# Kernel optimization log

Measured on AMD Instinct MI355X. Metric: run time of the kernel, lower is better.

Reference implementation:

```python
import jax, jax.numpy as jnp
import numpy as np

B, S, N = 16, 64, 4096
D = 64            # input_dim*seq_len == output_dim*graph_dim
FEAT = 64
E = 32768
HEADS = (3, 3, 1)
NEG_SLOPE = 0.2   # PyG GATConv default negative_slope


def _lin_init(key, fi, fo):
    k1, k2 = jax.random.split(key)
    s = 1.0 / np.sqrt(fi)
    return (jax.random.uniform(k1, (fi, fo), jnp.float32, -s, s),
            jax.random.uniform(k2, (fo,), jnp.float32, -s, s))


def setup_inputs() -> dict:
    key = jax.random.key(0)
    ks = jax.random.split(key, 32)
    inp = {}
    inp["inputs"] = jax.random.normal(ks[0], (B, S, N, 1), jnp.float32)
    inp["edge_index"] = jax.random.randint(ks[1], (2, E), 0, N, dtype=jnp.int32)
    inp["W_seq"], inp["b_seq"] = _lin_init(ks[2], D, D)
    inp["src_embed"] = jax.random.normal(ks[3], (N, FEAT), jnp.float32) * 0.1
    inp["tgt_embed"] = jax.random.normal(ks[4], (FEAT, N), jnp.float32) * 0.1
    for i, H in enumerate(HEADS):
        s = 1.0 / np.sqrt(D)
        inp[f"Wg{i}"] = jax.random.uniform(ks[5 + 5 * i], (D, H * D), jnp.float32, -s, s)
        inp[f"asrc{i}"] = jax.random.normal(ks[6 + 5 * i], (H, D), jnp.float32) * 0.1
        inp[f"adst{i}"] = jax.random.normal(ks[7 + 5 * i], (H, D), jnp.float32) * 0.1
        inp[f"bg{i}"] = jnp.zeros((D,), jnp.float32)
        inp[f"Wl{i}"], inp[f"bl{i}"] = _lin_init(ks[8 + 5 * i], D, D)
    inp["Wo"], inp["bo"] = _lin_init(ks[25], D, D)
    return inp


def _gat(x, src, dst, W, a_src, a_dst, b):
    # PyG GATConv, concat=False (mean over heads). x: [B,N,D] -> [B,N,D]
    H, C = a_src.shape
    xp = jnp.einsum('bnd,dhc->bnhc', x, W.reshape(D, H, C))       # [B,N,H,C]
    al_s = jnp.einsum('bnhc,hc->bnh', xp, a_src)
    al_d = jnp.einsum('bnhc,hc->bnh', xp, a_dst)
    e = jax.nn.leaky_relu(al_s[:, src] + al_d[:, dst], NEG_SLOPE)  # [B,Et,H]

    def per_graph(e_b, xj_b):
        m = jax.ops.segment_max(e_b, dst, num_segments=N)          # [N,H]
        w = jnp.exp(e_b - m[dst])
        z = jax.ops.segment_sum(w, dst, num_segments=N)
        alpha = w / z[dst]                                         # softmax per dst node
        return jax.ops.segment_sum(xj_b * alpha[..., None], dst, num_segments=N)

    out = jax.vmap(per_graph)(e, xp[:, src])                       # [B,N,H,C]
    return out.mean(axis=2) + b


def _forward(inputs, edge_index, W_seq, b_seq, src_embed, tgt_embed,
             Wg0, asrc0, adst0, bg0, Wl0, bl0,
             Wg1, asrc1, adst1, bg1, Wl1, bl1,
             Wg2, asrc2, adst2, bg2, Wl2, bl2, Wo, bo):
    loop = jnp.arange(N, dtype=edge_index.dtype)
    src = jnp.concatenate([edge_index[0], loop])   # PyG add_self_loops=True
    dst = jnp.concatenate([edge_index[1], loop])
    h = inputs.transpose(0, 2, 3, 1).reshape(B * N, D)
    h = h @ W_seq + b_seq + h                       # seq_linear residual
    A = jax.nn.softmax(jax.nn.relu(src_embed @ tgt_embed), axis=1)  # learned adjacency [N,N]
    gat_p = [(Wg0, asrc0, adst0, bg0), (Wg1, asrc1, adst1, bg1), (Wg2, asrc2, adst2, bg2)]
    lin_p = [(Wl0, bl0), (Wl1, bl1), (Wl2, bl2)]
    for i in range(3):
        hb = h.reshape(B, N, D)
        # layer-0 GAT output is computed but unused in the original code (dead); skip it
        h_cur = _gat(hb, src, dst, *gat_p[i]).reshape(B * N, D) if i > 0 else None
        adp = jnp.einsum('mn,bnd->bmd', A, hb)      # adaptive-graph matmul (dropout in eval = identity)
        adp = (adp @ lin_p[i][0] + lin_p[i][1]).reshape(B * N, D)
        g = jax.nn.sigmoid(adp)
        if i == 0:
            origin = h @ Wo + bo
            h = jnp.tanh(h) * g + origin * (1.0 - g)
        elif i == 1:
            h = jax.nn.leaky_relu(h_cur, 0.01) * g + h * (1.0 - g)
        else:
            h = jax.nn.relu(h_cur) * g + h * (1.0 - g)
    return h.reshape(B, N, 1, D)   # [batch, node_num, output_dim, graph_dim]


def reference(inputs, edge_index, W_seq, b_seq, src_embed, tgt_embed,
              Wg0, asrc0, adst0, bg0, Wl0, bl0,
              Wg1, asrc1, adst1, bg1, Wl1, bl1,
              Wg2, asrc2, adst2, bg2, Wl2, bl2, Wo, bo):
    return _forward(inputs, edge_index, W_seq, b_seq, src_embed, tgt_embed,
                    Wg0, asrc0, adst0, bg0, Wl0, bl0,
                    Wg1, asrc1, adst1, bg1, Wl1, bl1,
                    Wg2, asrc2, adst2, bg2, Wl2, bl2, Wo, bo)
```

## Files before the change

kernel.cpp:

```cpp
#include <hip/hip_runtime.h>
#include <stdint.h>

#define NB 16
#define NN 4096
#define DD 64
#define EE 32768
#define ETOT 36864
#define ROWS 65536
#define KSPLIT 4

typedef _Float16 f16;
typedef f16   half8 __attribute__((ext_vector_type(8)));
typedef f16   f16x8 __attribute__((ext_vector_type(8)));
typedef f16   f16x4 __attribute__((ext_vector_type(4)));
typedef float f32x4 __attribute__((ext_vector_type(4)));

__device__ __forceinline__ void gload16(const f16* g, f16* l) {
  __builtin_amdgcn_global_load_lds((const __attribute__((address_space(1))) void*)g,
                                   (__attribute__((address_space(3))) void*)l, 16, 0, 0);
}

__global__ __launch_bounds__(256) void k_zero2(int* a, int* b) {
  int i = blockIdx.x * 256 + threadIdx.x;
  if (i < NN) a[i] = 0;
  else if (i < 2 * NN) b[i - NN] = 0;
}

__global__ __launch_bounds__(256) void k_count(const int* __restrict__ ei, int* __restrict__ cnt) {
  int t = blockIdx.x * 256 + threadIdx.x;
  if (t >= ETOT) return;
  int d = (t < EE) ? ei[EE + t] : (t - EE);
  atomicAdd(&cnt[d], 1);
}

__global__ __launch_bounds__(256) void k_scan(const int* __restrict__ cnt, int* __restrict__ offs) {
  __shared__ int part[256];
  int t = threadIdx.x;
  int loc[16]; int s = 0;
  #pragma unroll
  for (int i = 0; i < 16; ++i) { int v = cnt[(t << 4) + i]; loc[i] = s; s += v; }
  part[t] = s;
  __syncthreads();
  int own = s;
  for (int d = 1; d < 256; d <<= 1) {
    int u = (t >= d) ? part[t - d] : 0;
    __syncthreads();
    part[t] += u;
    __syncthreads();
  }
  int base = part[t] - own;
  #pragma unroll
  for (int i = 0; i < 16; ++i) offs[(t << 4) + i] = base + loc[i];
}

__global__ __launch_bounds__(256) void k_fill(const int* __restrict__ ei, const int* __restrict__ offs,
                                              int* __restrict__ cur, int* __restrict__ esrc,
                                              int* __restrict__ edst) {
  int t = blockIdx.x * 256 + threadIdx.x;
  if (t >= ETOT) return;
  int s, d;
  if (t < EE) { s = ei[t]; d = ei[EE + t]; } else { s = d = t - EE; }
  int p = atomicAdd(&cur[d], 1);
  esrc[offs[d] + p] = s;
  edst[offs[d] + p] = d;
}

__global__ __launch_bounds__(256) void k_seq(const float* __restrict__ inp, const float* __restrict__ Wseq,
                                             const float* __restrict__ bseq, float* __restrict__ h) {
  __shared__ float X[64 * 68];
  int t = threadIdx.x;
  int b = blockIdx.x >> 6, n0 = (blockIdx.x & 63) << 6;
  #pragma unroll
  for (int i = 0; i < 16; ++i) {
    int idx = t + (i << 8);
    int s = idx >> 6, nl = idx & 63;
    X[nl * 68 + s] = inp[((size_t)((b << 6) + s) << 12) + n0 + nl];
  }
  __syncthreads();
  int c = t & 63, rg = t >> 6;
  float Wc[64];
  #pragma unroll
  for (int k = 0; k < 64; ++k) Wc[k] = Wseq[(k << 6) + c];
  float bc = bseq[c];
  for (int rr = 0; rr < 16; ++rr) {
    int r = (rg << 4) + rr;
    float a = bc + X[r * 68 + c];
    #pragma unroll
    for (int k4 = 0; k4 < 16; ++k4) {
      float4 x = *(const float4*)&X[r * 68 + (k4 << 2)];
      a = fmaf(x.x, Wc[4*k4+0], a); a = fmaf(x.y, Wc[4*k4+1], a);
      a = fmaf(x.z, Wc[4*k4+2], a); a = fmaf(x.w, Wc[4*k4+3], a);
    }
    h[((size_t)(b << 12) + n0 + r) * 64 + c] = a;
  }
}

__global__ __launch_bounds__(256) void k_adjmm(const f16* __restrict__ SEh, const f16* __restrict__ TEh,
                                               f16* __restrict__ A, float* __restrict__ Zpart) {
  __shared__ f16 Al[2][128 * 32];
  __shared__ f16 Bl[2][128 * 32];
  const int t = threadIdx.x, lane = t & 63, w = t >> 6;
  const int m0 = blockIdx.y << 7, j0 = blockIdx.x << 7;
  const int l15 = lane & 15, lhi = lane >> 4;
  const int wm = (w >> 1) << 6, wj = (w & 1) << 6;
  f32x4 acc[4][4] = {};
  const int c0 = (w << 6) + lane;
  const int row0 = c0 >> 2, ko0 = (c0 & 3) << 3;
  const int c1 = c0 + 256;
  const int row1 = c1 >> 2, ko1 = (c1 & 3) << 3;
  const f16* ga0 = SEh + (size_t)(m0 + row0) * 64 + ko0;
  const f16* ga1 = SEh + (size_t)(m0 + row1) * 64 + ko1;
  const f16* gb0 = TEh + (size_t)(j0 + row0) * 64 + ko0;
  const f16* gb1 = TEh + (size_t)(j0 + row1) * 64 + ko1;
  #pragma unroll
  for (int kt = 0; kt < 2; ++kt) {
    const int kof = kt << 5;
    gload16(ga0 + kof, Al[kt] + c0 * 8);
    gload16(ga1 + kof, Al[kt] + c1 * 8);
    gload16(gb0 + kof, Bl[kt] + c0 * 8);
    gload16(gb1 + kof, Bl[kt] + c1 * 8);
  }
  __syncthreads();
  #pragma unroll
  for (int kt = 0; kt < 2; ++kt) {
    half8 af[4], bf[4];
    #pragma unroll
    for (int i = 0; i < 4; ++i) {
      af[i] = *(const half8*)(Al[kt] + (wm + i * 16 + l15) * 32 + lhi * 8);
      bf[i] = *(const half8*)(Bl[kt] + (wj + i * 16 + l15) * 32 + lhi * 8);
    }
    #pragma unroll
    for (int mi = 0; mi < 4; ++mi)
      #pragma unroll
      for (int nj = 0; nj < 4; ++nj)
        acc[mi][nj] = __builtin_amdgcn_mfma_f32_16x16x32_f16(af[mi], bf[nj], acc[mi][nj], 0, 0, 0);
  }
  float rs[4][4];
  #pragma unroll
  for (int mi = 0; mi < 4; ++mi)
    #pragma unroll
    for (int r = 0; r < 4; ++r) rs[mi][r] = 0.f;
  #pragma unroll
  for (int mi = 0; mi < 4; ++mi)
    #pragma unroll
    for (int nj = 0; nj < 4; ++nj)
      #pragma unroll
      for (int r = 0; r < 4; ++r) {
        int row = m0 + wm + mi * 16 + lhi * 4 + r;
        int col = j0 + wj + nj * 16 + l15;
        float e = __expf(fmaxf(acc[mi][nj][r], 0.f));
        f16 eh = (f16)e;
        A[((size_t)row << 12) + col] = eh;
        rs[mi][r] += (float)eh;
      }
  #pragma unroll
  for (int mi = 0; mi < 4; ++mi)
    #pragma unroll
    for (int r = 0; r < 4; ++r) {
      float s = rs[mi][r];
      s += __shfl_xor(s, 1); s += __shfl_xor(s, 2);
      s += __shfl_xor(s, 4); s += __shfl_xor(s, 8);
      rs[mi][r] = s;
    }
  if (l15 == 0) {
    int p = (blockIdx.x << 1) + (w & 1);
    #pragma unroll
    for (int mi = 0; mi < 4; ++mi)
      #pragma unroll
      for (int r = 0; r < 4; ++r)
        Zpart[((size_t)p << 12) + m0 + wm + mi * 16 + lhi * 4 + r] = rs[mi][r];
  }
}

__global__ __launch_bounds__(256) void k_rowz(const float* __restrict__ Zpart, float* __restrict__ rowZ) {
  int row = blockIdx.x * 256 + threadIdx.x;
  float s = 0.f;
  #pragma unroll 8
  for (int p = 0; p < 64; ++p) s += Zpart[((size_t)p << 12) + row];
  rowZ[row] = 1.f / s;
}

#define NKT 16
__global__ __launch_bounds__(512) void k_gemm8(const f16* __restrict__ A, const f16* __restrict__ BT,
                                               f16* __restrict__ Cout) {
  extern __shared__ f16 smem[];
  const int t = threadIdx.x, lane = t & 63, wid = t >> 6;
  const int wr = wid >> 2, wc = wid & 3;
  const int l15 = lane & 15, lhi = lane >> 4;
  const int h7 = l15 & 7;
  const int wgid = blockIdx.x;
  const int nid = (wgid & 7) * 32 + (wgid >> 3);
  const int z = nid >> 6, rem = nid & 63;
  const int m0 = (rem >> 2) << 8;
  const int j0 = (rem & 3) << 8;
  const size_t kbase = (size_t)z << 10;
  f16* __restrict__ Cz = Cout + ((size_t)z << 22);

  const f16* gA[4]; int lA[4];
  #pragma unroll
  for (int i = 0; i < 4; ++i) {
    int s = t + (i << 9), row = s >> 3, sl = (s & 7) ^ (row & 7);
    gA[i] = A + (size_t)(m0 + row) * 4096 + kbase + sl * 8;
    lA[i] = s * 8;
  }
  const f16* gB[4]; int lB[4];
  #pragma unroll
  for (int i = 0; i < 4; ++i) {
    int s = t + (i << 9), row = s >> 3, sl = (s & 7) ^ (row & 7);
    gB[i] = BT + (size_t)(j0 + row) * 4096 + kbase + sl * 8;
    lB[i] = 16384 + s * 8;
  }
  #define SA(buf, kt, i) gload16(gA[i] + (kt) * 64, smem + (buf) * 32768 + lA[i])
  #define SB(buf, kt, i) gload16(gB[i] + (kt) * 64, smem + (buf) * 32768 + lB[i])

  const int rbase = wr << 7;
  const int cbase = wc << 6;
  f32x4 acc[8][4] = {};

  #pragma unroll
  for (int i = 0; i < 4; ++i) SA(0, 0, i);
  #pragma unroll
  for (int i = 0; i < 4; ++i) SB(0, 0, i);
  asm volatile("s_waitcnt vmcnt(0)" ::: "memory");
  __builtin_amdgcn_sched_barrier(0);
  __builtin_amdgcn_s_barrier();
  __builtin_amdgcn_sched_barrier(0);

  for (int kt = 0; kt < NKT; ++kt) {
    const int cur = kt & 1;
    const f16* Ab = smem + cur * 32768;
    const f16* Bb = Ab + 16384;
    const bool pf = (kt + 1 < NKT);
    {
      half8 af[8], bf[4];
      #pragma unroll
      for (int mi = 0; mi < 8; ++mi) {
        int row = rbase + mi * 16 + l15;
        af[mi] = *(const half8*)(Ab + row * 64 + (lhi ^ h7) * 8);
      }
      #pragma unroll
      for (int nj = 0; nj < 4; ++nj) {
        int row = cbase + nj * 16 + l15;
        bf[nj] = *(const half8*)(Bb + row * 64 + (lhi ^ h7) * 8);
      }
      if (pf) { SA(cur ^ 1, kt + 1, 0); SA(cur ^ 1, kt + 1, 1); SA(cur ^ 1, kt + 1, 2); SA(cur ^ 1, kt + 1, 3); }
      __builtin_amdgcn_s_setprio(1);
      #pragma unroll
      for (int mi = 0; mi < 8; ++mi)
        #pragma unroll
        for (int nj = 0; nj < 4; ++nj)
          acc[mi][nj] = __builtin_amdgcn_mfma_f32_16x16x32_f16(af[mi], bf[nj], acc[mi][nj], 0, 0, 0);
      __builtin_amdgcn_s_setprio(0);
    }
    {
      half8 af[8], bf[4];
      #pragma unroll
      for (int mi = 0; mi < 8; ++mi) {
        int row = rbase + mi * 16 + l15;
        af[mi] = *(const half8*)(Ab + row * 64 + ((4 + lhi) ^ h7) * 8);
      }
      #pragma unroll
      for (int nj = 0; nj < 4; ++nj) {
        int row = cbase + nj * 16 + l15;
        bf[nj] = *(const half8*)(Bb + row * 64 + ((4 + lhi) ^ h7) * 8);
      }
      if (pf) { SB(cur ^ 1, kt + 1, 0); SB(cur ^ 1, kt + 1, 1); SB(cur ^ 1, kt + 1, 2); SB(cur ^ 1, kt + 1, 3); }
      __builtin_amdgcn_s_setprio(1);
      #pragma unroll
      for (int mi = 0; mi < 8; ++mi)
        #pragma unroll
        for (int nj = 0; nj < 4; ++nj)
          acc[mi][nj] = __builtin_amdgcn_mfma_f32_16x16x32_f16(af[mi], bf[nj], acc[mi][nj], 0, 0, 0);
      __builtin_amdgcn_s_setprio(0);
    }
    if (pf) {
      asm volatile("s_waitcnt vmcnt(0)" ::: "memory");
      __builtin_amdgcn_sched_barrier(0);
      __builtin_amdgcn_s_barrier();
      __builtin_amdgcn_sched_barrier(0);
    }
  }
  #undef SA
  #undef SB
  #pragma unroll
  for (int mi = 0; mi < 8; ++mi)
    #pragma unroll
    for (int nj = 0; nj < 4; ++nj)
      #pragma unroll
      for (int r = 0; r < 4; ++r) {
        int row = m0 + rbase + mi * 16 + (lhi << 2) + r;
        int col = j0 + cbase + nj * 16 + l15;
        Cz[(size_t)row * 1024 + col] = (f16)acc[mi][nj][r];
      }
}

template<int H, int NP>
__device__ __forceinline__ void wprep_body(const float* __restrict__ Wg, const float* __restrict__ asrc,
                                           const float* __restrict__ adst, const float* __restrict__ Wl,
                                           f16* __restrict__ Wgh, int bid, int t) {
  const int WL0 = H * 64 + 16;
  for (int i = bid * 256 + t; i < NP * 64; i += 16 * 256) {
    int j = i >> 6, k = i & 63;
    float v;
    if (j < H * 64) {
      v = Wg[(size_t)k * (H * 64) + j];
    } else if (j < H * 64 + 2 * H) {
      int cc = j - H * 64, hh = cc >> 1;
      const float* a = ((cc & 1) ? adst : asrc) + (hh << 6);
      const float* wrow = Wg + (size_t)k * (H * 64) + (hh << 6);
      float s = 0.f;
      #pragma unroll 16
      for (int c = 0; c < 64; ++c) s = fmaf(wrow[c], a[c], s);
      v = s;
    } else if (j >= WL0 && j < WL0 + 64) {
      v = Wl[(k << 6) + (j - WL0)];
    } else v = 0.f;
    Wgh[(size_t)j * 64 + k] = (f16)v;
  }
}

__global__ __launch_bounds__(256) void k_allprep(
    const float* __restrict__ Wg1, const float* __restrict__ as1, const float* __restrict__ ad1,
    const float* __restrict__ Wl1, f16* __restrict__ Wgh1,
    const float* __restrict__ Wg2, const float* __restrict__ as2, const float* __restrict__ ad2,
    const float* __restrict__ Wl2, f16* __restrict__ Wgh2,
    const float* __restrict__ Wl0, const float* __restrict__ Wo, f16* __restrict__ W0h,
    const float* __restrict__ SE, const float* __restrict__ TE,
    f16* __restrict__ SEh, f16* __restrict__ TEh) {
  __shared__ float X[64 * 65];
  int bid = blockIdx.x, t = threadIdx.x;
  if (bid < 16) { wprep_body<3, 272>(Wg1, as1, ad1, Wl1, Wgh1, bid, t); return; }
  if (bid < 32) { wprep_body<1, 144>(Wg2, as2, ad2, Wl2, Wgh2, bid - 16, t); return; }
  if (bid < 40) {
    for (int i = (bid - 32) * 256 + t; i < 128 * 64; i += 8 * 256) {
      int j = i >> 6, k = i & 63;
      float v = (j < 64) ? Wl0[(k << 6) + j] : Wo[(k << 6) + (j - 64)];
      W0h[(size_t)j * 64 + k] = (f16)v;
    }
    return;
  }
  if (bid < 296) {
    int i = ((bid - 40) * 256 + t) * 4;
    float4 v = *(const float4*)(SE + i);
    f16 o[4] = {(f16)v.x, (f16)v.y, (f16)v.z, (f16)v.w};
    *(uint64_t*)(SEh + i) = *(uint64_t*)o;
    return;
  }
  int j0 = (bid - 296) << 6;
  #pragma unroll
  for (int i = 0; i < 16; ++i) {
    int idx = t + (i << 8);
    int k = idx >> 6, jl = idx & 63;
    X[jl * 65 + k] = TE[((size_t)k << 12) + j0 + jl];
  }
  __syncthreads();
  int jl = t >> 2, kg = t & 3;
  f16 o[16];
  #pragma unroll
  for (int i = 0; i < 16; ++i) o[i] = (f16)X[jl * 65 + (kg << 4) + i];
  f16* dst = TEh + ((size_t)(j0 + jl) << 6) + (kg << 4);
  *(uint64_t*)(dst + 0) = *(uint64_t*)(o + 0);
  *(uint64_t*)(dst + 4) = *(uint64_t*)(o + 4);
  *(uint64_t*)(dst + 8) = *(uint64_t*)(o + 8);
  *(uint64_t*)(dst + 12) = *(uint64_t*)(o + 12);
}

template<int H, int NP>
__global__ __launch_bounds__(256) void k_xpmm(const float* __restrict__ h, const f16* __restrict__ Wgh,
                                              f16* __restrict__ xp, float* __restrict__ als,
                                              float* __restrict__ ald, f16* __restrict__ HWlT) {
  const int WL0 = H * 64 + 16, JW0 = WL0 / 16, NT = NP / 16;
  __shared__ f16 Ah[64 * 72];
  __shared__ f16 Bh[NP * 72];
  __shared__ f16 stage[64 * 72];
  const int t = threadIdx.x, lane = t & 63, w = t >> 6;
  const size_t r0 = (size_t)blockIdx.x * 64;
  const int b = (int)(r0 >> 12), n0 = (int)(r0 & 4095);
  #pragma unroll
  for (int i = 0; i < 4; ++i) {
    int idx = t + (i << 8);
    int row = idx >> 4, k4 = (idx & 15) << 2;
    float4 v = *(const float4*)&h[(r0 + row) * 64 + k4];
    f16 o[4] = {(f16)v.x, (f16)v.y, (f16)v.z, (f16)v.w};
    *(uint64_t*)&Ah[row * 72 + k4] = *(uint64_t*)o;
  }
  for (int i = t; i < NP * 16; i += 256) {
    int row = i >> 4, k4 = (i & 15) << 2;
    *(uint64_t*)&Bh[row * 72 + k4] = *(const uint64_t*)&Wgh[(size_t)row * 64 + k4];
  }
  __syncthreads();
  const int l15 = lane & 15, lhi = lane >> 4;
  f32x4 acc[NT] = {};
  #pragma unroll
  for (int kk = 0; kk < 2; ++kk) {
    half8 af = *(const half8*)&Ah[(w * 16 + l15) * 72 + kk * 32 + lhi * 8];
    #pragma unroll
    for (int j = 0; j < NT; ++j) {
      half8 bf = *(const half8*)&Bh[(j * 16 + l15) * 72 + kk * 32 + lhi * 8];
      acc[j] = __builtin_amdgcn_mfma_f32_16x16x32_f16(af, bf, acc[j], 0, 0, 0);
    }
  }
  const int rl = w * 16 + lhi * 4;
  #pragma unroll
  for (int j = 0; j < NT; ++j) {
    int col = j * 16 + l15;
    if (j * 16 + 15 < H * 64) {
      #pragma unroll
      for (int r = 0; r < 4; ++r) {
        if (H == 3) xp[(r0 + rl + r) * 256 + ((col & 63) << 2) + (col >> 6)] = (f16)acc[j][r];
        else        xp[(r0 + rl + r) * 64 + col] = (f16)acc[j][r];
      }
    } else if (j < JW0) {
      int cc = col - H * 64;
      if (cc >= 0 && cc < 2 * H) {
        int hh = cc >> 1;
        #pragma unroll
        for (int r = 0; r < 4; ++r) {
          if (cc & 1) ald[(r0 + rl + r) * H + hh] = acc[j][r];
          else        als[(r0 + rl + r) * H + hh] = acc[j][r];
        }
      }
    } else {
      int e = col - WL0;
      f16 o[4] = {(f16)acc[j][0], (f16)acc[j][1], (f16)acc[j][2], (f16)acc[j][3]};
      *(uint64_t*)&stage[e * 72 + rl] = *(uint64_t*)o;
    }
  }
  __syncthreads();
  {
    int e = t >> 2, seg = (t & 3) << 4;
    float4 v0 = *(const float4*)&stage[e * 72 + seg];
    float4 v1 = *(const float4*)&stage[e * 72 + seg + 8];
    f16* dst = HWlT + (((size_t)((b << 6) + e)) << 12) + n0 + seg;
    *(float4*)dst = v0;
    *(float4*)(dst + 8) = v1;
  }
}

__global__ __launch_bounds__(256) void k_prep0(const float* __restrict__ h, const f16* __restrict__ W0h,
                                               f16* __restrict__ HWlT, f16* __restrict__ orig) {
  __shared__ f16 Ah[64 * 72];
  __shared__ f16 Bh[128 * 72];
  __shared__ f16 stage[64 * 72];
  const int t = threadIdx.x, lane = t & 63, w = t >> 6;
  const size_t r0 = (size_t)blockIdx.x * 64;
  const int b = (int)(r0 >> 12), n0 = (int)(r0 & 4095);
  #pragma unroll
  for (int i = 0; i < 4; ++i) {
    int idx = t + (i << 8);
    int row = idx >> 4, k4 = (idx & 15) << 2;
    float4 v = *(const float4*)&h[(r0 + row) * 64 + k4];
    f16 o[4] = {(f16)v.x, (f16)v.y, (f16)v.z, (f16)v.w};
    *(uint64_t*)&Ah[row * 72 + k4] = *(uint64_t*)o;
  }
  for (int i = t; i < 128 * 16; i += 256) {
    int row = i >> 4, k4 = (i & 15) << 2;
    *(uint64_t*)&Bh[row * 72 + k4] = *(const uint64_t*)&W0h[(size_t)row * 64 + k4];
  }
  __syncthreads();
  const int l15 = lane & 15, lhi = lane >> 4;
  f32x4 acc[8] = {};
  #pragma unroll
  for (int kk = 0; kk < 2; ++kk) {
    half8 af = *(const half8*)&Ah[(w * 16 + l15) * 72 + kk * 32 + lhi * 8];
    #pragma unroll
    for (int j = 0; j < 8; ++j) {
      half8 bf = *(const half8*)&Bh[(j * 16 + l15) * 72 + kk * 32 + lhi * 8];
      acc[j] = __builtin_amdgcn_mfma_f32_16x16x32_f16(af, bf, acc[j], 0, 0, 0);
    }
  }
  const int rl = w * 16 + lhi * 4;
  #pragma unroll
  for (int j = 0; j < 8; ++j) {
    int col = j * 16 + l15;
    if (j < 4) {
      f16 o[4] = {(f16)acc[j][0], (f16)acc[j][1], (f16)acc[j][2], (f16)acc[j][3]};
      *(uint64_t*)&stage[col * 72 + rl] = *(uint64_t*)o;
    } else {
      #pragma unroll
      for (int r = 0; r < 4; ++r)
        orig[(r0 + rl + r) * 64 + (col - 64)] = (f16)acc[j][r];
    }
  }
  __syncthreads();
  {
    int e = t >> 2, seg = (t & 3) << 4;
    float4 v0 = *(const float4*)&stage[e * 72 + seg];
    float4 v1 = *(const float4*)&stage[e * 72 + seg + 8];
    f16* dst = HWlT + (((size_t)((b << 6) + e)) << 12) + n0 + seg;
    *(float4*)dst = v0;
    *(float4*)(dst + 8) = v1;
  }
}

template<int H>
__global__ __launch_bounds__(256) void k_maxals(const float* __restrict__ als, float* __restrict__ Mals) {
  __shared__ float red[256];
  int b = blockIdx.x, t = threadIdx.x;
  size_t rbase = (size_t)b << 12;
  for (int h = 0; h < H; ++h) {
    float m = -1e30f;
    for (int n = t; n < NN; n += 256) m = fmaxf(m, als[(rbase + n) * H + h]);
    red[t] = m;
    __syncthreads();
    for (int d = 128; d; d >>= 1) {
      if (t < d) red[t] = fmaxf(red[t], red[t + d]);
      __syncthreads();
    }
    if (t == 0) Mals[b * H + h] = red[0];
    __syncthreads();
  }
}

template<int H>
__global__ __launch_bounds__(256) void k_wts(const float* __restrict__ als, const float* __restrict__ ald,
                                             const float* __restrict__ Mals, const int* __restrict__ esrc,
                                             const int* __restrict__ edst, float* __restrict__ wts) {
  const int WST = (H == 3) ? 4 : 1;
  int t = threadIdx.x, lane = t & 63, w = t >> 6;
  int gw = blockIdx.x * 4 + w;
  int b = gw & 15;
  int p = ((gw >> 4) << 6) + lane;
  size_t rbase = (size_t)b << 12;
  int s = esrc[p], n = edst[p];
  float* dst = wts + ((size_t)b * ETOT + p) * WST;
  #pragma unroll
  for (int h = 0; h < H; ++h) {
    float ad = ald[(rbase + n) * H + h];
    float B = Mals[b * H + h] + ad;
    float T = B > 0.f ? B : 0.2f * B;
    float ev = als[(rbase + s) * H + h] + ad;
    ev = ev > 0.f ? ev : 0.2f * ev;
    dst[h] = __expf(ev - T);
  }
}

template<int H, int ACT>
__global__ __launch_bounds__(256) void k_aggc(const f16* __restrict__ xp, const float* __restrict__ wts,
                                              const int* __restrict__ offs, const int* __restrict__ cnt,
                                              const int* __restrict__ esrc, const float* __restrict__ bg,
                                              const float* __restrict__ h, const f16* __restrict__ gp,
                                              const float* __restrict__ rowZ, const float* __restrict__ bl,
                                              float* __restrict__ hout) {
  const int WST = (H == 3) ? 4 : 1;
  __shared__ float wbuf[4][64 * WST];
  __shared__ int   sbuf[4][64];
  int t = threadIdx.x, lane = t & 63, wv = t >> 6;
  int blk = blockIdx.x;
  int b = ((blk & 7) << 1) | ((blk >> 3) & 1);
  int n = ((blk >> 4) << 2) + wv;
  size_t rbase = (size_t)b << 12;
  int o = offs[n], c = cnt[n];
  const float* wsrc = wts + ((size_t)b * ETOT + o) * WST;
  float z[H], acc[H];
  #pragma unroll
  for (int hh = 0; hh < H; ++hh) { z[hh] = 0.f; acc[hh] = 0.f; }
  for (int e0 = 0; e0 < c; e0 += 64) {
    int ce = min(64, c - e0);
    if (lane < ce) {
      sbuf[wv][lane] = esrc[o + e0 + lane];
      if (H == 3) *(float4*)&wbuf[wv][lane * 4] = *(const float4*)&wsrc[(size_t)(e0 + lane) * 4];
      else        wbuf[wv][lane] = wsrc[e0 + lane];
    }
    #pragma unroll 4
    for (int e = 0; e < ce; ++e) {
      int s = sbuf[wv][e];
      if (H == 3) {
        float4 w4 = *(const float4*)&wbuf[wv][e * 4];
        f16x4 q = *(const f16x4*)(xp + (((size_t)(rbase + s)) << 8) + (lane << 2));
        z[0] += w4.x; acc[0] = fmaf(w4.x, (float)q[0], acc[0]);
        z[1] += w4.y; acc[1] = fmaf(w4.y, (float)q[1], acc[1]);
        z[2] += w4.z; acc[2] = fmaf(w4.z, (float)q[2], acc[2]);
      } else {
        float wv_ = wbuf[wv][e];
        float xv = (float)xp[(((size_t)(rbase + s)) << 6) + lane];
        z[0] += wv_; acc[0] = fmaf(wv_, xv, acc[0]);
      }
    }
  }
  float r = 0.f;
  #pragma unroll
  for (int hh = 0; hh < H; ++hh) r += acc[hh] / z[hh];
  float cv = r * (1.f / H) + bg[lane];
  size_t ga = ((size_t)n << 10) + (b << 6) + lane;
  float zi = rowZ[n];
  float gs = 0.f;
  #pragma unroll
  for (int p = 0; p < KSPLIT; ++p) gs += (float)gp[ga + (size_t)p * (4096 * 1024)];
  float g = 1.f / (1.f + __expf(-(gs * zi + bl[lane])));
  size_t ridx = ((rbase + n) << 6) + lane;
  float hv = h[ridx];
  float act = ACT ? fmaxf(cv, 0.f) : (cv > 0.f ? cv : 0.01f * cv);
  hout[ridx] = act * g + hv * (1.f - g);
}

__global__ __launch_bounds__(256) void k_comb0e(const float* __restrict__ h, const f16* __restrict__ gp,
                                                const float* __restrict__ rowZ, const f16* __restrict__ orig,
                                                const float* __restrict__ bl, const float* __restrict__ bo,
                                                float* __restrict__ hout) {
  for (size_t i4 = (size_t)blockIdx.x * 256 + threadIdx.x; i4 < (size_t)ROWS * 16; i4 += (size_t)2048 * 256) {
    size_t i = i4 * 4;
    int d = (int)(i & 63), n = (int)((i >> 6) & 4095), b = (int)(i >> 18);
    size_t ga = ((size_t)n << 10) + (b << 6) + d;
    float zi = rowZ[n];
    float gs[4] = {0.f, 0.f, 0.f, 0.f};
    #pragma unroll
    for (int p = 0; p < KSPLIT; ++p) {
      f16x4 gq = *(const f16x4*)&gp[ga + (size_t)p * (4096 * 1024)];
      gs[0] += (float)gq[0]; gs[1] += (float)gq[1]; gs[2] += (float)gq[2]; gs[3] += (float)gq[3];
    }
    f16x4 og = *(const f16x4*)&orig[i];
    float4 hv = *(const float4*)&h[i];
    float4 o;
    float* op = &o.x;
    const float* hp = &hv.x;
    #pragma unroll
    for (int r = 0; r < 4; ++r) {
      float g = 1.f / (1.f + __expf(-(gs[r] * zi + bl[d + r])));
      float orv = (float)og[r] + bo[d + r];
      op[r] = tanhf(hp[r]) * g + orv * (1.f - g);
    }
    *(float4*)&hout[i] = o;
  }
}

extern "C" void kernel_launch(void* const* d_in, const int* in_sizes, int n_in,
                              void* d_out, int out_size, void* d_ws, size_t ws_size,
                              hipStream_t stream) {
  (void)in_sizes; (void)n_in; (void)out_size; (void)ws_size;
  const float* inp  = (const float*)d_in[0];
  const int*   ei   = (const int*)d_in[1];
  const float* Wseq = (const float*)d_in[2];
  const float* bseq = (const float*)d_in[3];
  const float* SE   = (const float*)d_in[4];
  const float* TE   = (const float*)d_in[5];
  const float* Wg[3]   = {(const float*)d_in[6],  (const float*)d_in[12], (const float*)d_in[18]};
  const float* asrc[3] = {(const float*)d_in[7],  (const float*)d_in[13], (const float*)d_in[19]};
  const float* adst[3] = {(const float*)d_in[8],  (const float*)d_in[14], (const float*)d_in[20]};
  const float* bgp[3]  = {(const float*)d_in[9],  (const float*)d_in[15], (const float*)d_in[21]};
  const float* Wl[3]   = {(const float*)d_in[10], (const float*)d_in[16], (const float*)d_in[22]};
  const float* bl[3]   = {(const float*)d_in[11], (const float*)d_in[17], (const float*)d_in[23]};
  const float* Wo = (const float*)d_in[24];
  const float* bo = (const float*)d_in[25];
  float* out = (float*)d_out;

  uint8_t* ws = (uint8_t*)d_ws;
  size_t o = 0;
  auto nxt = [&](size_t sz) { void* p = ws + o; o += (sz + 255) & ~(size_t)255; return p; };
  f16*   Af   = (f16*)  nxt((size_t)NN * NN * sizeof(f16));
  f16*   HWlT = (f16*)  nxt((size_t)1024 * NN * sizeof(f16));
  float* h    = (float*)nxt((size_t)ROWS * 64 * 4);
  f16*   gp   = (f16*)  nxt((size_t)KSPLIT * NN * 1024 * sizeof(f16));
  f16*   xp   = (f16*)  nxt((size_t)ROWS * 256 * sizeof(f16));
  f16*   orig = (f16*)  nxt((size_t)ROWS * 64 * sizeof(f16));
  float* als  = (float*)nxt((size_t)ROWS * 3 * 4);
  float* ald  = (float*)nxt((size_t)ROWS * 3 * 4);
  float* rowZ = (float*)nxt((size_t)NN * 4);
  float* Zpart= (float*)nxt((size_t)64 * NN * 4);
  f16*   SEh  = (f16*)  nxt((size_t)NN * 64 * sizeof(f16));
  f16*   TEh  = (f16*)  nxt((size_t)NN * 64 * sizeof(f16));
  f16*   Wgh1 = (f16*)  nxt((size_t)288 * 64 * sizeof(f16));
  f16*   Wgh2 = (f16*)  nxt((size_t)144 * 64 * sizeof(f16));
  f16*   W0h  = (f16*)  nxt((size_t)128 * 64 * sizeof(f16));
  float* wts  = (float*)nxt((size_t)NB * ETOT * 4 * 4);
  float* Mals = (float*)nxt((size_t)NB * 3 * 4);
  int*   cnt  = (int*)  nxt((size_t)NN * 4);
  int*   curp = (int*)  nxt((size_t)NN * 4);
  int*   offs = (int*)  nxt((size_t)NN * 4);
  int*   esrc = (int*)  nxt((size_t)ETOT * 4);
  int*   edst = (int*)  nxt((size_t)ETOT * 4);

  static bool attr_set = false;
  if (!attr_set) {
    hipFuncSetAttribute((const void*)k_gemm8, hipFuncAttributeMaxDynamicSharedMemorySize, 131072);
    attr_set = true;
  }

  dim3 blk(256);
  k_zero2<<<32, blk, 0, stream>>>(cnt, curp);
  k_count<<<144, blk, 0, stream>>>(ei, cnt);
  k_scan<<<1, blk, 0, stream>>>(cnt, offs);
  k_fill<<<144, blk, 0, stream>>>(ei, offs, curp, esrc, edst);
  k_allprep<<<360, blk, 0, stream>>>(Wg[1], asrc[1], adst[1], Wl[1], Wgh1,
                                     Wg[2], asrc[2], adst[2], Wl[2], Wgh2,
                                     Wl[0], Wo, W0h, SE, TE, SEh, TEh);
  k_seq<<<1024, blk, 0, stream>>>(inp, Wseq, bseq, h);
  k_adjmm<<<dim3(32, 32), blk, 0, stream>>>(SEh, TEh, Af, Zpart);
  k_rowz<<<16, blk, 0, stream>>>(Zpart, rowZ);
  k_prep0<<<1024, blk, 0, stream>>>(h, W0h, HWlT, orig);
  k_gemm8<<<256, 512, 131072, stream>>>(Af, HWlT, gp);
  k_comb0e<<<2048, blk, 0, stream>>>(h, gp, rowZ, orig, bl[0], bo, h);
  k_xpmm<3, 272><<<1024, blk, 0, stream>>>(h, Wgh1, xp, als, ald, HWlT);
  k_maxals<3><<<16, blk, 0, stream>>>(als, Mals);
  k_wts<3><<<2304, blk, 0, stream>>>(als, ald, Mals, esrc, edst, wts);
  k_gemm8<<<256, 512, 131072, stream>>>(Af, HWlT, gp);
  k_aggc<3, 0><<<16384, blk, 0, stream>>>(xp, wts, offs, cnt, esrc, bgp[1], h, gp, rowZ, bl[1], h);
  k_xpmm<1, 144><<<1024, blk, 0, stream>>>(h, Wgh2, xp, als, ald, HWlT);
  k_maxals<1><<<16, blk, 0, stream>>>(als, Mals);
  k_wts<1><<<2304, blk, 0, stream>>>(als, ald, Mals, esrc, edst, wts);
  k_gemm8<<<256, 512, 131072, stream>>>(Af, HWlT, gp);
  k_aggc<1, 1><<<16384, blk, 0, stream>>>(xp, wts, offs, cnt, esrc, bgp[2], h, gp, rowZ, bl[2], out);
}
```

Measured before the change: 302.0 us.

## Fuse GAT edge-weight computation into aggregation kernel, drop max and weights passes

Removes the separate per-graph max-reduction and edge-weight kernels. Attention logits are now computed inside the aggregation kernel from padded 4-wide als/ald arrays, with exp clamped at 60 in place of subtracting a global max. This avoids writing and reading a large per-edge weight buffer, the edst array and two launches per layer. It also uses readfirstlane for the source index. The trade-off is that the unshifted exp relies on the clamp for range, which could lose precision or overflow-protect differently for large logits.

```diff
diff --git a/kernel.cpp b/kernel.cpp
--- a/kernel.cpp
+++ b/kernel.cpp
@@ -54,15 +54,13 @@
 }
 
 __global__ __launch_bounds__(256) void k_fill(const int* __restrict__ ei, const int* __restrict__ offs,
-                                              int* __restrict__ cur, int* __restrict__ esrc,
-                                              int* __restrict__ edst) {
+                                              int* __restrict__ cur, int* __restrict__ esrc) {
   int t = blockIdx.x * 256 + threadIdx.x;
   if (t >= ETOT) return;
   int s, d;
   if (t < EE) { s = ei[t]; d = ei[EE + t]; } else { s = d = t - EE; }
   int p = atomicAdd(&cur[d], 1);
   esrc[offs[d] + p] = s;
-  edst[offs[d] + p] = d;
 }
 
 __global__ __launch_bounds__(256) void k_seq(const float* __restrict__ inp, const float* __restrict__ Wseq,
@@ -367,8 +365,8 @@
 
 template<int H, int NP>
 __global__ __launch_bounds__(256) void k_xpmm(const float* __restrict__ h, const f16* __restrict__ Wgh,
-                                              f16* __restrict__ xp, float* __restrict__ als,
-                                              float* __restrict__ ald, f16* __restrict__ HWlT) {
+                                              f16* __restrict__ xp, float* __restrict__ als4,
+                                              float* __restrict__ ald4, f16* __restrict__ HWlT) {
   const int WL0 = H * 64 + 16, JW0 = WL0 / 16, NT = NP / 16;
   __shared__ f16 Ah[64 * 72];
   __shared__ f16 Bh[NP * 72];
@@ -416,8 +414,8 @@
         int hh = cc >> 1;
         #pragma unroll
         for (int r = 0; r < 4; ++r) {
-          if (cc & 1) ald[(r0 + rl + r) * H + hh] = acc[j][r];
-          else        als[(r0 + rl + r) * H + hh] = acc[j][r];
+          if (cc & 1) ald4[(r0 + rl + r) * 4 + hh] = acc[j][r];
+          else        als4[(r0 + rl + r) * 4 + hh] = acc[j][r];
         }
       }
     } else {
@@ -493,50 +491,9 @@
   }
 }
 
-template<int H>
-__global__ __launch_bounds__(256) void k_maxals(const float* __restrict__ als, float* __restrict__ Mals) {
-  __shared__ float red[256];
-  int b = blockIdx.x, t = threadIdx.x;
-  size_t rbase = (size_t)b << 12;
-  for (int h = 0; h < H; ++h) {
-    float m = -1e30f;
-    for (int n = t; n < NN; n += 256) m = fmaxf(m, als[(rbase + n) * H + h]);
-    red[t] = m;
-    __syncthreads();
-    for (int d = 128; d; d >>= 1) {
-      if (t < d) red[t] = fmaxf(red[t], red[t + d]);
-      __syncthreads();
-    }
-    if (t == 0) Mals[b * H + h] = red[0];
-    __syncthreads();
-  }
-}
-
-template<int H>
-__global__ __launch_bounds__(256) void k_wts(const float* __restrict__ als, const float* __restrict__ ald,
-                                             const float* __restrict__ Mals, const int* __restrict__ esrc,
-                                             const int* __restrict__ edst, float* __restrict__ wts) {
-  const int WST = (H == 3) ? 4 : 1;
-  int t = threadIdx.x, lane = t & 63, w = t >> 6;
-  int gw = blockIdx.x * 4 + w;
-  int b = gw & 15;
-  int p = ((gw >> 4) << 6) + lane;
-  size_t rbase = (size_t)b << 12;
-  int s = esrc[p], n = edst[p];
-  float* dst = wts + ((size_t)b * ETOT + p) * WST;
-  #pragma unroll
-  for (int h = 0; h < H; ++h) {
-    float ad = ald[(rbase + n) * H + h];
-    float B = Mals[b * H + h] + ad;
-    float T = B > 0.f ? B : 0.2f * B;
-    float ev = als[(rbase + s) * H + h] + ad;
-    ev = ev > 0.f ? ev : 0.2f * ev;
-    dst[h] = __expf(ev - T);
-  }
-}
-
 template<int H, int ACT>
-__global__ __launch_bounds__(256) void k_aggc(const f16* __restrict__ xp, const float* __restrict__ wts,
+__global__ __launch_bounds__(256) void k_aggc(const f16* __restrict__ xp, const float* __restrict__ als4,
+                                              const float* __restrict__ ald4,
                                               const int* __restrict__ offs, const int* __restrict__ cnt,
                                               const int* __restrict__ esrc, const float* __restrict__ bg,
                                               const float* __restrict__ h, const f16* __restrict__ gp,
@@ -551,29 +508,47 @@
   int n = ((blk >> 4) << 2) + wv;
   size_t rbase = (size_t)b << 12;
   int o = offs[n], c = cnt[n];
-  const float* wsrc = wts + ((size_t)b * ETOT + o) * WST;
+  float ad0 = ald4[(rbase + n) * 4 + 0];
+  float ad1 = (H == 3) ? ald4[(rbase + n) * 4 + 1] : 0.f;
+  float ad2 = (H == 3) ? ald4[(rbase + n) * 4 + 2] : 0.f;
+  const f16* xpb = xp + (rbase << (H == 3 ? 8 : 6));
   float z[H], acc[H];
   #pragma unroll
   for (int hh = 0; hh < H; ++hh) { z[hh] = 0.f; acc[hh] = 0.f; }
   for (int e0 = 0; e0 < c; e0 += 64) {
     int ce = min(64, c - e0);
     if (lane < ce) {
-      sbuf[wv][lane] = esrc[o + e0 + lane];
-      if (H == 3) *(float4*)&wbuf[wv][lane * 4] = *(const float4*)&wsrc[(size_t)(e0 + lane) * 4];
-      else        wbuf[wv][lane] = wsrc[e0 + lane];
+      int sl = esrc[o + e0 + lane];
+      sbuf[wv][lane] = sl;
+      if (H == 3) {
+        float4 a4 = *(const float4*)&als4[(rbase + sl) * 4];
+        float ev0 = a4.x + ad0; ev0 = ev0 > 0.f ? ev0 : 0.2f * ev0;
+        float ev1 = a4.y + ad1; ev1 = ev1 > 0.f ? ev1 : 0.2f * ev1;
+        float ev2 = a4.z + ad2; ev2 = ev2 > 0.f ? ev2 : 0.2f * ev2;
+        float4 w4;
+        w4.x = __expf(fminf(ev0, 60.f));
+        w4.y = __expf(fminf(ev1, 60.f));
+        w4.z = __expf(fminf(ev2, 60.f));
+        w4.w = 0.f;
+        *(float4*)&wbuf[wv][lane * 4] = w4;
+      } else {
+        float ev = als4[(rbase + sl) * 4] + ad0;
+        ev = ev > 0.f ? ev : 0.2f * ev;
+        wbuf[wv][lane] = __expf(fminf(ev, 60.f));
+      }
     }
     #pragma unroll 4
     for (int e = 0; e < ce; ++e) {
-      int s = sbuf[wv][e];
+      int s = __builtin_amdgcn_readfirstlane(sbuf[wv][e]);
       if (H == 3) {
         float4 w4 = *(const float4*)&wbuf[wv][e * 4];
-        f16x4 q = *(const f16x4*)(xp + (((size_t)(rbase + s)) << 8) + (lane << 2));
+        f16x4 q = *(const f16x4*)(xpb + ((size_t)s << 8) + (lane << 2));
         z[0] += w4.x; acc[0] = fmaf(w4.x, (float)q[0], acc[0]);
         z[1] += w4.y; acc[1] = fmaf(w4.y, (float)q[1], acc[1]);
         z[2] += w4.z; acc[2] = fmaf(w4.z, (float)q[2], acc[2]);
       } else {
         float wv_ = wbuf[wv][e];
-        float xv = (float)xp[(((size_t)(rbase + s)) << 6) + lane];
+        float xv = (float)xpb[((size_t)s << 6) + lane];
         z[0] += wv_; acc[0] = fmaf(wv_, xv, acc[0]);
       }
     }
@@ -653,8 +628,8 @@
   f16*   gp   = (f16*)  nxt((size_t)KSPLIT * NN * 1024 * sizeof(f16));
   f16*   xp   = (f16*)  nxt((size_t)ROWS * 256 * sizeof(f16));
   f16*   orig = (f16*)  nxt((size_t)ROWS * 64 * sizeof(f16));
-  float* als  = (float*)nxt((size_t)ROWS * 3 * 4);
-  float* ald  = (float*)nxt((size_t)ROWS * 3 * 4);
+  float* als4 = (float*)nxt((size_t)ROWS * 4 * 4);
+  float* ald4 = (float*)nxt((size_t)ROWS * 4 * 4);
   float* rowZ = (float*)nxt((size_t)NN * 4);
   float* Zpart= (float*)nxt((size_t)64 * NN * 4);
   f16*   SEh  = (f16*)  nxt((size_t)NN * 64 * sizeof(f16));
@@ -662,13 +637,10 @@
   f16*   Wgh1 = (f16*)  nxt((size_t)288 * 64 * sizeof(f16));
   f16*   Wgh2 = (f16*)  nxt((size_t)144 * 64 * sizeof(f16));
   f16*   W0h  = (f16*)  nxt((size_t)128 * 64 * sizeof(f16));
-  float* wts  = (float*)nxt((size_t)NB * ETOT * 4 * 4);
-  float* Mals = (float*)nxt((size_t)NB * 3 * 4);
   int*   cnt  = (int*)  nxt((size_t)NN * 4);
   int*   curp = (int*)  nxt((size_t)NN * 4);
   int*   offs = (int*)  nxt((size_t)NN * 4);
   int*   esrc = (int*)  nxt((size_t)ETOT * 4);
-  int*   edst = (int*)  nxt((size_t)ETOT * 4);
 
   static bool attr_set = false;
   if (!attr_set) {
@@ -680,7 +652,7 @@
   k_zero2<<<32, blk, 0, stream>>>(cnt, curp);
   k_count<<<144, blk, 0, stream>>>(ei, cnt);
   k_scan<<<1, blk, 0, stream>>>(cnt, offs);
-  k_fill<<<144, blk, 0, stream>>>(ei, offs, curp, esrc, edst);
+  k_fill<<<144, blk, 0, stream>>>(ei, offs, curp, esrc);
   k_allprep<<<360, blk, 0, stream>>>(Wg[1], asrc[1], adst[1], Wl[1], Wgh1,
                                      Wg[2], asrc[2], adst[2], Wl[2], Wgh2,
                                      Wl[0], Wo, W0h, SE, TE, SEh, TEh);
@@ -690,14 +662,10 @@
   k_prep0<<<1024, blk, 0, stream>>>(h, W0h, HWlT, orig);
   k_gemm8<<<256, 512, 131072, stream>>>(Af, HWlT, gp);
   k_comb0e<<<2048, blk, 0, stream>>>(h, gp, rowZ, orig, bl[0], bo, h);
-  k_xpmm<3, 272><<<1024, blk, 0, stream>>>(h, Wgh1, xp, als, ald, HWlT);
-  k_maxals<3><<<16, blk, 0, stream>>>(als, Mals);
-  k_wts<3><<<2304, blk, 0, stream>>>(als, ald, Mals, esrc, edst, wts);
+  k_xpmm<3, 272><<<1024, blk, 0, stream>>>(h, Wgh1, xp, als4, ald4, HWlT);
   k_gemm8<<<256, 512, 131072, stream>>>(Af, HWlT, gp);
-  k_aggc<3, 0><<<16384, blk, 0, stream>>>(xp, wts, offs, cnt, esrc, bgp[1], h, gp, rowZ, bl[1], h);
-  k_xpmm<1, 144><<<1024, blk, 0, stream>>>(h, Wgh2, xp, als, ald, HWlT);
-  k_maxals<1><<<16, blk, 0, stream>>>(als, Mals);
-  k_wts<1><<<2304, blk, 0, stream>>>(als, ald, Mals, esrc, edst, wts);
+  k_aggc<3, 0><<<16384, blk, 0, stream>>>(xp, als4, ald4, offs, cnt, esrc, bgp[1], h, gp, rowZ, bl[1], h);
+  k_xpmm<1, 144><<<1024, blk, 0, stream>>>(h, Wgh2, xp, als4, ald4, HWlT);
   k_gemm8<<<256, 512, 131072, stream>>>(Af, HWlT, gp);
-  k_aggc<1, 1><<<16384, blk, 0, stream>>>(xp, wts, offs, cnt, esrc, bgp[2], h, gp, rowZ, bl[2], out);
-}
+  k_aggc<1, 1><<<16384, blk, 0, stream>>>(xp, als4, ald4, offs, cnt, esrc, bgp[2], h, gp, rowZ, bl[2], out);
+}
```

Result: slower. 308.4 us (+2.1%).
